# Optimization experiments

Hardware: AMD Instinct MI355X
Metric: run time of the kernel (lower is better)

Reference implementation:

```python
import jax, jax.numpy as jnp
import numpy as np

NUM_ROUTING_ITERATIONS = 3


def _squash(t, axis=-1):
    # scale * t / ||t||, scale = ||t||^2 / (1 + ||t||^2)
    squared_norm = jnp.sum(t * t, axis=axis, keepdims=True)
    return squared_norm / (1.0 + squared_norm) * t / jnp.sqrt(squared_norm)


def setup_inputs() -> dict:
    key = jax.random.key(0)
    k_x, k_w = jax.random.split(key)
    B, R, C, O, I = 64, 2048, 16, 32, 16
    x = jax.random.normal(k_x, (B, R, I), dtype=jnp.float32)
    W = jax.random.normal(k_w, (R, C, O, I), dtype=jnp.float32)
    return {"x": x, "W": W}


def reference(x, W):
    # u_hat[b,r,c,o] = sum_i W[r,c,o,i] * x[b,r,i]
    u_hat = jnp.einsum('rcoi,bri->brco', W, x)  # [B,R,C,O]
    B, R, C, O = u_hat.shape
    b = jnp.zeros((B, R, C), dtype=u_hat.dtype)  # routing logits
    v = None
    for _ in range(NUM_ROUTING_ITERATIONS):
        c = jax.nn.softmax(b, axis=2)                      # softmax over capsules (dim=2)
        s = jnp.einsum('brc,brco->bro', c, u_hat)          # (c * u_hat).sum(dim=2)
        v = _squash(s, axis=-1)                            # [B,R,O]
        b = b + jnp.einsum('brco,bro->brc', u_hat, v)      # agreement update
    return v
```

## Files before the change

### kernel.cpp

```cpp
#include <hip/hip_runtime.h>

#define R_DIM 2048
#define O_DIM 32
#define I_DIM 16
#define B_DIM 64
#define BB 16

typedef _Float16 half8  __attribute__((ext_vector_type(8)));
typedef float    f32x4  __attribute__((ext_vector_type(4)));

struct SplitH { half8 h1, h2; };

__device__ __forceinline__ SplitH splitf16x8(const float* __restrict__ p) {
    float f[8];
    *(float4*)(f)     = *(const float4*)(p);
    *(float4*)(f + 4) = *(const float4*)(p + 4);
    SplitH r;
    #pragma unroll
    for (int j = 0; j < 4; ++j) {
        const auto a = __builtin_amdgcn_cvt_pkrtz(f[2*j], f[2*j+1]);
        const float r0 = f[2*j]     - (float)a[0];
        const float r1 = f[2*j + 1] - (float)a[1];
        const auto c = __builtin_amdgcn_cvt_pkrtz(r0, r1);
        r.h1[2*j] = (_Float16)a[0]; r.h1[2*j+1] = (_Float16)a[1];
        r.h2[2*j] = (_Float16)c[0]; r.h2[2*j+1] = (_Float16)c[1];
    }
    return r;
}

template<int CTRL>
__device__ __forceinline__ float dpp_mv(float v) {
    int t = __builtin_amdgcn_update_dpp(0, __float_as_int(v), CTRL, 0xf, 0xf, true);
    return __int_as_float(t);
}
__device__ __forceinline__ float row16_sum(float v) {
    v += dpp_mv<0xB1>(v);
    v += dpp_mv<0x4E>(v);
    v += dpp_mv<0x124>(v);
    v += dpp_mv<0x128>(v);
    return v;
}
__device__ __forceinline__ float row16_max(float v) {
    v = fmaxf(v, dpp_mv<0xB1>(v));
    v = fmaxf(v, dpp_mv<0x4E>(v));
    v = fmaxf(v, dpp_mv<0x124>(v));
    v = fmaxf(v, dpp_mv<0x128>(v));
    return v;
}
__device__ __forceinline__ float ror1(float v) { return dpp_mv<0x121>(v); }

__device__ __forceinline__ int swaddr(int b, int col) {
    return b * 512 + (col ^ (((b ^ (b >> 2)) & 3) << 3));
}

__global__ __launch_bounds__(512, 8)
void capsule_routing_kernel(const float* __restrict__ x,
                            const float* __restrict__ W,
                            float* __restrict__ out) {
    __shared__ float u_lds[BB * 512];

    const int tid = threadIdx.x;
    const int bid = blockIdx.x;
    const int r   = bid >> 2;
    const int b0  = (bid & 3) * BB;

    {
        const int lane = tid & 63;
        const int w    = tid >> 6;
        const int q    = lane >> 4;
        const int np   = lane & 15;

        const half8 z8 = {0,0,0,0,0,0,0,0};
        SplitH as; as.h1 = z8; as.h2 = z8;
        if (q < 2)
            as = splitf16x8(x + ((size_t)(b0 + np) * R_DIM + r) * I_DIM + q * 8);

        const f32x4 zero4 = {0.f, 0.f, 0.f, 0.f};
        #pragma unroll
        for (int t = 0; t < 4; ++t) {
            const int ntile = w * 4 + t;
            SplitH bs; bs.h1 = z8; bs.h2 = z8;
            if (q < 2)
                bs = splitf16x8(W + ((size_t)r * 512 + ntile * 16 + np) * I_DIM + q * 8);

            f32x4 a = __builtin_amdgcn_mfma_f32_16x16x32_f16(as.h2, bs.h1, zero4, 0, 0, 0);
            a = __builtin_amdgcn_mfma_f32_16x16x32_f16(as.h1, bs.h2, a, 0, 0, 0);
            a = __builtin_amdgcn_mfma_f32_16x16x32_f16(as.h1, bs.h1, a, 0, 0, 0);

            const int col = ntile * 16 + np;
            #pragma unroll
            for (int reg = 0; reg < 4; ++reg)
                u_lds[swaddr(q * 4 + reg, col)] = a[reg];
        }
    }
    __syncthreads();

    if (tid < 256) {
        const int b = tid >> 4;
        const int j = tid & 15;

        float u2[32];
        #pragma unroll
        for (int k = 0; k < 16; ++k) {
            const int c = (j - k) & 15;
            const float2 v2 = *(const float2*)&u_lds[swaddr(b, c * 32 + 2 * j)];
            u2[2 * k]     = v2.x;
            u2[2 * k + 1] = v2.y;
        }

        float bvv = 0.0f;
        float s0 = 0.f, s1 = 0.f, g = 0.f;

        #pragma unroll
        for (int it = 0; it < 3; ++it) {
            if (it == 0) {
                s0 = 0.f; s1 = 0.f;
                #pragma unroll
                for (int k = 0; k < 16; ++k) { s0 += u2[2*k]; s1 += u2[2*k+1]; }
                s0 *= 0.0625f; s1 *= 0.0625f;
            } else {
                const float m = row16_max(bvv);
                const float e = __expf(bvv - m);
                const float Z = row16_sum(e);
                float wr = e * __builtin_amdgcn_rcpf(Z);
                s0 = 0.f; s1 = 0.f;
                #pragma unroll
                for (int k = 0; k < 16; ++k) {
                    if (k > 0) wr = ror1(wr);
                    s0 = fmaf(wr, u2[2*k],     s0);
                    s1 = fmaf(wr, u2[2*k + 1], s1);
                }
            }

            const float nn = row16_sum(s0 * s0 + s1 * s1);
            g = sqrtf(nn) * __builtin_amdgcn_rcpf(1.0f + nn);

            if (it < 2) {
                float acc = 0.f;
                #pragma unroll
                for (int k = 0; k < 16; ++k) {
                    if (k > 0) acc = ror1(acc);
                    acc = fmaf(u2[2*k],     s0, acc);
                    acc = fmaf(u2[2*k + 1], s1, acc);
                }
                acc = ror1(acc);
                bvv = fmaf(g, acc, bvv);
            }
        }

        *(float2*)(out + ((size_t)(b0 + b) * R_DIM + r) * O_DIM + 2 * j)
            = make_float2(g * s0, g * s1);
    }
}

extern "C" void kernel_launch(void* const* d_in, const int* in_sizes, int n_in,
                              void* d_out, int out_size, void* d_ws, size_t ws_size,
                              hipStream_t stream) {
    const float* x   = (const float*)d_in[0];
    const float* W   = (const float*)d_in[1];
    float*       out = (float*)d_out;

    dim3 grid(R_DIM * (B_DIM / BB));
    dim3 block(512);
    hipLaunchKernelGGL(capsule_routing_kernel, grid, block, 0, stream, x, W, out);
}
```

Before: 138.5 us.

## Use 16x16x16 MFMA without padding, remap blocks by r groups, split routing rotation chains

Switches from the 16x16x32 f16 MFMA, where half the lanes loaded zeros, to the 16x16x16 variant so every lane loads a useful float4 of x and W. Block indices are remapped so that consecutive blocks cover 8 adjacent routes for one batch slice. The intended gain is better L2/cache locality for x and W. The routing loops are split into two independent accumulator chains stepped by ror2, which halves the dependent DPP chain length. It also simplifies LDS address computation with a precomputed swizzle, at the risk of subtle indexing errors in the rotation bookkeeping.

```diff
diff --git a/kernel.cpp b/kernel.cpp
--- a/kernel.cpp
+++ b/kernel.cpp
@@ -6,26 +6,23 @@
 #define B_DIM 64
 #define BB 16
 
-typedef _Float16 half8  __attribute__((ext_vector_type(8)));
+typedef _Float16 half4  __attribute__((ext_vector_type(4)));
 typedef float    f32x4  __attribute__((ext_vector_type(4)));
 
-struct SplitH { half8 h1, h2; };
+struct SplitH4 { half4 h1, h2; };
 
-__device__ __forceinline__ SplitH splitf16x8(const float* __restrict__ p) {
-    float f[8];
-    *(float4*)(f)     = *(const float4*)(p);
-    *(float4*)(f + 4) = *(const float4*)(p + 4);
-    SplitH r;
-    #pragma unroll
-    for (int j = 0; j < 4; ++j) {
-        const auto a = __builtin_amdgcn_cvt_pkrtz(f[2*j], f[2*j+1]);
-        const float r0 = f[2*j]     - (float)a[0];
-        const float r1 = f[2*j + 1] - (float)a[1];
-        const auto c = __builtin_amdgcn_cvt_pkrtz(r0, r1);
-        r.h1[2*j] = (_Float16)a[0]; r.h1[2*j+1] = (_Float16)a[1];
-        r.h2[2*j] = (_Float16)c[0]; r.h2[2*j+1] = (_Float16)c[1];
-    }
-    return r;
+__device__ __forceinline__ SplitH4 splitf16x4(const float* __restrict__ p) {
+    const float4 f = *(const float4*)p;
+    const auto a0 = __builtin_amdgcn_cvt_pkrtz(f.x, f.y);
+    const auto a1 = __builtin_amdgcn_cvt_pkrtz(f.z, f.w);
+    const auto c0 = __builtin_amdgcn_cvt_pkrtz(f.x - (float)a0[0], f.y - (float)a0[1]);
+    const auto c1 = __builtin_amdgcn_cvt_pkrtz(f.z - (float)a1[0], f.w - (float)a1[1]);
+    SplitH4 s;
+    s.h1[0] = (_Float16)a0[0]; s.h1[1] = (_Float16)a0[1];
+    s.h1[2] = (_Float16)a1[0]; s.h1[3] = (_Float16)a1[1];
+    s.h2[0] = (_Float16)c0[0]; s.h2[1] = (_Float16)c0[1];
+    s.h2[2] = (_Float16)c1[0]; s.h2[3] = (_Float16)c1[1];
+    return s;
 }
 
 template<int CTRL>
@@ -48,10 +45,7 @@
     return v;
 }
 __device__ __forceinline__ float ror1(float v) { return dpp_mv<0x121>(v); }
-
-__device__ __forceinline__ int swaddr(int b, int col) {
-    return b * 512 + (col ^ (((b ^ (b >> 2)) & 3) << 3));
-}
+__device__ __forceinline__ float ror2(float v) { return dpp_mv<0x122>(v); }
 
 __global__ __launch_bounds__(512, 8)
 void capsule_routing_kernel(const float* __restrict__ x,
@@ -61,8 +55,8 @@
 
     const int tid = threadIdx.x;
     const int bid = blockIdx.x;
-    const int r   = bid >> 2;
-    const int b0  = (bid & 3) * BB;
+    const int r   = ((bid >> 5) << 3) | (bid & 7);
+    const int b0  = ((bid >> 3) & 3) * BB;
 
     {
         const int lane = tid & 63;
@@ -70,27 +64,27 @@
         const int q    = lane >> 4;
         const int np   = lane & 15;
 
-        const half8 z8 = {0,0,0,0,0,0,0,0};
-        SplitH as; as.h1 = z8; as.h2 = z8;
-        if (q < 2)
-            as = splitf16x8(x + ((size_t)(b0 + np) * R_DIM + r) * I_DIM + q * 8);
+        const SplitH4 as = splitf16x4(x + ((size_t)(b0 + np) * R_DIM + r) * I_DIM + q * 4);
+
+        const float* Wbase = W + (size_t)r * 8192 + (size_t)(w * 4) * 256 + np * 16 + q * 4;
 
         const f32x4 zero4 = {0.f, 0.f, 0.f, 0.f};
         #pragma unroll
         for (int t = 0; t < 4; ++t) {
             const int ntile = w * 4 + t;
-            SplitH bs; bs.h1 = z8; bs.h2 = z8;
-            if (q < 2)
-                bs = splitf16x8(W + ((size_t)r * 512 + ntile * 16 + np) * I_DIM + q * 8);
+            const SplitH4 bs = splitf16x4(Wbase + t * 256);
 
-            f32x4 a = __builtin_amdgcn_mfma_f32_16x16x32_f16(as.h2, bs.h1, zero4, 0, 0, 0);
-            a = __builtin_amdgcn_mfma_f32_16x16x32_f16(as.h1, bs.h2, a, 0, 0, 0);
-            a = __builtin_amdgcn_mfma_f32_16x16x32_f16(as.h1, bs.h1, a, 0, 0, 0);
+            f32x4 a = __builtin_amdgcn_mfma_f32_16x16x16f16(as.h2, bs.h1, zero4, 0, 0, 0);
+            a = __builtin_amdgcn_mfma_f32_16x16x16f16(as.h1, bs.h2, a, 0, 0, 0);
+            a = __builtin_amdgcn_mfma_f32_16x16x16f16(as.h1, bs.h1, a, 0, 0, 0);
 
             const int col = ntile * 16 + np;
-            #pragma unroll
-            for (int reg = 0; reg < 4; ++reg)
-                u_lds[swaddr(q * 4 + reg, col)] = a[reg];
+            const int v0  = col ^ (q << 3);
+            float* pb = u_lds + q * 2048;
+            pb[v0]               = a[0];
+            pb[512  + (v0 ^ 8)]  = a[1];
+            pb[1024 + (v0 ^ 16)] = a[2];
+            pb[1536 + (v0 ^ 24)] = a[3];
         }
     }
     __syncthreads();
@@ -99,13 +93,17 @@
         const int b = tid >> 4;
         const int j = tid & 15;
 
-        float u2[32];
-        #pragma unroll
-        for (int k = 0; k < 16; ++k) {
-            const int c = (j - k) & 15;
-            const float2 v2 = *(const float2*)&u_lds[swaddr(b, c * 32 + 2 * j)];
-            u2[2 * k]     = v2.x;
-            u2[2 * k + 1] = v2.y;
+        const int sw = ((b ^ (b >> 2)) & 3) << 3;
+        const float* pb = u_lds + b * 512 + ((2 * j) ^ sw);
+
+        float2 u2p[16];
+        {
+            int c = j;
+            #pragma unroll
+            for (int k = 0; k < 16; ++k) {
+                u2p[k] = *(const float2*)&pb[c * 32];
+                c = (c - 1) & 15;
+            }
         }
 
         float bvv = 0.0f;
@@ -116,34 +114,41 @@
             if (it == 0) {
                 s0 = 0.f; s1 = 0.f;
                 #pragma unroll
-                for (int k = 0; k < 16; ++k) { s0 += u2[2*k]; s1 += u2[2*k+1]; }
+                for (int k = 0; k < 16; ++k) { s0 += u2p[k].x; s1 += u2p[k].y; }
                 s0 *= 0.0625f; s1 *= 0.0625f;
             } else {
-                const float m = row16_max(bvv);
-                const float e = __expf(bvv - m);
-                const float Z = row16_sum(e);
-                float wr = e * __builtin_amdgcn_rcpf(Z);
-                s0 = 0.f; s1 = 0.f;
+                const float mx = row16_max(bvv);
+                const float e  = __expf(bvv - mx);
+                const float Z  = row16_sum(e);
+                float wA = e * __builtin_amdgcn_rcpf(Z);
+                float wB = ror1(wA);
+                float sA0 = 0.f, sA1 = 0.f, sB0 = 0.f, sB1 = 0.f;
                 #pragma unroll
-                for (int k = 0; k < 16; ++k) {
-                    if (k > 0) wr = ror1(wr);
-                    s0 = fmaf(wr, u2[2*k],     s0);
-                    s1 = fmaf(wr, u2[2*k + 1], s1);
+                for (int m = 0; m < 8; ++m) {
+                    if (m) { wA = ror2(wA); wB = ror2(wB); }
+                    sA0 = fmaf(wA, u2p[2 * m].x,     sA0);
+                    sA1 = fmaf(wA, u2p[2 * m].y,     sA1);
+                    sB0 = fmaf(wB, u2p[2 * m + 1].x, sB0);
+                    sB1 = fmaf(wB, u2p[2 * m + 1].y, sB1);
                 }
+                s0 = sA0 + sB0;
+                s1 = sA1 + sB1;
             }
 
-            const float nn = row16_sum(s0 * s0 + s1 * s1);
+            const float nn = row16_sum(fmaf(s0, s0, s1 * s1));
             g = sqrtf(nn) * __builtin_amdgcn_rcpf(1.0f + nn);
 
             if (it < 2) {
-                float acc = 0.f;
+                float accA = 0.f, accB = 0.f;
                 #pragma unroll
-                for (int k = 0; k < 16; ++k) {
-                    if (k > 0) acc = ror1(acc);
-                    acc = fmaf(u2[2*k],     s0, acc);
-                    acc = fmaf(u2[2*k + 1], s1, acc);
+                for (int m = 0; m < 8; ++m) {
+                    if (m) { accA = ror2(accA); accB = ror2(accB); }
+                    accA = fmaf(u2p[2 * m].x,     s0, accA);
+                    accA = fmaf(u2p[2 * m].y,     s1, accA);
+                    accB = fmaf(u2p[2 * m + 1].x, s0, accB);
+                    accB = fmaf(u2p[2 * m + 1].y, s1, accB);
                 }
-                acc = ror1(acc);
+                const float acc = ror2(accA) + ror1(accB);
                 bvv = fmaf(g, acc, bvv);
             }
         }
```

Measured after the change: 120.0 us. -13.4%, faster.
